# Performance work log

Measured on AMD Instinct MI355X. Metric: run time of the kernel, lower is better.

The kernel has to match this reference:

```python
import jax, jax.numpy as jnp
import numpy as np

B, S, D = 4, 2048, 2048
D_INNER = max(128, D // 2)  # 1024, torch default d_inner
FO = 2                      # filter_order
K = 3                       # kernel_size
KS = 3                      # short_kernel_size


def setup_inputs() -> dict:
    key = jax.random.key(0)
    ks = jax.random.split(key, 6)
    return {
        "x": jax.random.normal(ks[0], (B, S, D), jnp.float32),
        # depthwise short conv: weight (D, KS), bias (D,)
        "short_w": jax.random.normal(ks[1], (D, KS), jnp.float32) / np.float32(np.sqrt(KS)),
        "short_b": jnp.zeros((D,), jnp.float32),
        # filter MLP proj: Linear(D -> FO*D_INNER)
        "proj_w": jax.random.normal(ks[2], (D, FO * D_INNER), jnp.float32) / np.float32(np.sqrt(D)),
        "proj_b": jnp.zeros((FO * D_INNER,), jnp.float32),
        # filter MLP output: Linear(D_INNER -> K), SHARED across filter orders
        "filt_w": jax.random.normal(ks[3], (D_INNER, K), jnp.float32) / np.float32(np.sqrt(D_INNER)),
        "filt_b": jnp.zeros((K,), jnp.float32),
        # output projection Linear(D -> D)
        "out_w": jax.random.normal(ks[4], (D, D), jnp.float32) / np.float32(np.sqrt(D)),
        "out_b": jnp.zeros((D,), jnp.float32),
    }


def reference(x, short_w, short_b, proj_w, proj_b, filt_w, filt_b, out_w, out_b):
    b, s, d = x.shape
    v = x  # v captured BEFORE short-conv residual, as in the torch code

    # --- causal depthwise short conv (pad k-1 on left, truncate to s) ---
    xp = jnp.pad(x, ((0, 0), (KS - 1, 0), (0, 0)))
    x_short = short_b
    for j in range(KS):  # tiny fixed kernel loop
        x_short = x_short + xp[:, j:j + s, :] * short_w[:, j]
    x = x + x_short

    # --- filter function: Linear -> GELU -> (shared) Linear -> tanh ---
    h = jax.nn.gelu(x @ proj_w + proj_b, approximate=False)         # (b, s, FO*D_INNER)
    h = h.reshape(b, s, FO, D_INNER)
    filt = jnp.tanh(jnp.einsum('bsfi,ik->bsfk', h, filt_w) + filt_b)  # (b, s, FO, K)

    # --- gated depthwise conv: kernel = mean over seq, shared across channels;
    # sum over filter orders commutes with the (linear) conv, so fold it in ---
    w = filt.mean(axis=1).sum(axis=1)                                # (b, K)
    xp2 = jnp.pad(x, ((0, 0), (K - 1, 0), (0, 0)))
    conv = jnp.zeros_like(x)
    for j in range(K):
        conv = conv + xp2[:, j:j + s, :] * w[:, j][:, None, None]

    # --- gate with v, GELU, output projection ---
    y = jax.nn.gelu(conv * v, approximate=False)
    return y @ out_w + out_b
```

## Files before the change

kernel.cpp:

```cpp
#include <hip/hip_runtime.h>
#include <hip/hip_bf16.h>
#include <math.h>

typedef unsigned short u16;
typedef __attribute__((ext_vector_type(4))) unsigned short u16x4;
typedef __attribute__((ext_vector_type(8))) unsigned short u16x8;
typedef __attribute__((ext_vector_type(8))) short s16x8;
typedef __attribute__((ext_vector_type(4))) float f32x4;

#define B_  4
#define S_  2048
#define D_  2048
#define DI_ 1024
#define MROWS (B_ * S_)
#define KDIM  D_
#define NDIM  D_

__device__ __forceinline__ float b2f(u16 u) {
    union { unsigned i; float f; } v; v.i = ((unsigned)u) << 16; return v.f;
}
__device__ __forceinline__ u16 f2b(float f) {
    unsigned u = __float_as_uint(f);
    unsigned r = (u + 0x7FFFu + ((u >> 16) & 1u)) >> 16;
    return (u16)r;
}
__device__ __forceinline__ float gelu_exact(float x) {
    return 0.5f * x * (1.0f + erff(x * 0.70710678118654752f));
}

#define GLOAD_LDS16(gp, lp)                                                    \
    __builtin_amdgcn_global_load_lds(                                          \
        (const __attribute__((address_space(1))) void*)(gp),                   \
        (__attribute__((address_space(3))) void*)(lp), 16, 0, 0)

__global__ void transpose_k(const float* __restrict__ in, u16* __restrict__ out, int n) {
    __shared__ float tile[32][33];
    int bx = blockIdx.x * 32, by = blockIdx.y * 32;
    int tx = threadIdx.x, ty = threadIdx.y;
    for (int i = 0; i < 32; i += 8)
        tile[ty + i][tx] = in[(size_t)(by + ty + i) * n + bx + tx];
    __syncthreads();
    for (int i = 0; i < 32; i += 8)
        out[(size_t)(bx + ty + i) * n + by + tx] = f2b(tile[tx][ty + i]);
}

__global__ void shortconv_k(const float* __restrict__ x, const float* __restrict__ sw,
                            const float* __restrict__ sb, u16* __restrict__ xs,
                            float* __restrict__ wacc) {
    if (blockIdx.x == 0 && threadIdx.x < 12) wacc[threadIdx.x] = 0.0f;
    int gid = blockIdx.x * 256 + threadIdx.x;
    int r = gid >> 9;
    int c = (gid & 511) << 2;
    int t = r & (S_ - 1);
    const float* base = x + (size_t)r * D_ + c;
    f32x4 cur = *(const f32x4*)base;
    f32x4 m1 = (t >= 1) ? *(const f32x4*)(base - D_) : (f32x4)(0.0f);
    f32x4 m2 = (t >= 2) ? *(const f32x4*)(base - 2 * D_) : (f32x4)(0.0f);
    u16x4 out;
    #pragma unroll
    for (int e = 0; e < 4; ++e) {
        int d = c + e;
        float v = cur[e] + sb[d]
                + sw[d * 3 + 0] * m2[e]
                + sw[d * 3 + 1] * m1[e]
                + sw[d * 3 + 2] * cur[e];
        out[e] = f2b(v);
    }
    *(u16x4*)(xs + (size_t)r * D_ + c) = out;
}

template <bool GELU, bool OUT_F32>
__global__ void gemm_k(const u16* __restrict__ A, const u16* __restrict__ BT,
                       const float* __restrict__ bias, void* __restrict__ Cv,
                       int M, int N, int K) {
    __shared__ u16 As[128 * 32];
    __shared__ u16 Bs[128 * 32];
    const int tid = threadIdx.x;
    const int wid = tid >> 6;
    const int lane = tid & 63;
    const int wm = (wid >> 1) * 64;
    const int wn = (wid & 1) * 64;
    const int row0 = blockIdx.y * 128;
    const int col0 = blockIdx.x * 128;

    f32x4 acc[4][4];
    #pragma unroll
    for (int i = 0; i < 4; ++i)
        #pragma unroll
        for (int j = 0; j < 4; ++j) acc[i][j] = (f32x4)(0.0f);

    const int srow_l = lane >> 2;
    const int sk = (lane & 3) * 8;

    const int mrow = wm + (lane & 15);
    const int nrow = wn + (lane & 15);
    const int k0 = (lane >> 4) * 8;

    for (int kt = 0; kt < K; kt += 32) {
        __syncthreads();
        #pragma unroll
        for (int p = 0; p < 2; ++p) {
            int srow = p * 64 + wid * 16 + srow_l;
            u16* lpa = &As[(p * 4 + wid) * 512];
            u16* lpb = &Bs[(p * 4 + wid) * 512];
            const u16* ga = A + (size_t)(row0 + srow) * K + kt + sk;
            const u16* gb = BT + (size_t)(col0 + srow) * K + kt + sk;
            GLOAD_LDS16(ga, lpa);
            GLOAD_LDS16(gb, lpb);
        }
        __syncthreads();

        s16x8 af[4], bfr[4];
        #pragma unroll
        for (int i = 0; i < 4; ++i)
            af[i] = *(const s16x8*)&As[(size_t)(mrow + i * 16) * 32 + k0];
        #pragma unroll
        for (int j = 0; j < 4; ++j)
            bfr[j] = *(const s16x8*)&Bs[(size_t)(nrow + j * 16) * 32 + k0];
        #pragma unroll
        for (int i = 0; i < 4; ++i)
            #pragma unroll
            for (int j = 0; j < 4; ++j)
                acc[i][j] = __builtin_amdgcn_mfma_f32_16x16x32_bf16(
                    af[i], bfr[j], acc[i][j], 0, 0, 0);
    }

    const int crow0 = row0 + wm + (lane >> 4) * 4;
    const int ccol0 = col0 + wn + (lane & 15);
    #pragma unroll
    for (int j = 0; j < 4; ++j) {
        int col = ccol0 + j * 16;
        float bs = bias[col];
        #pragma unroll
        for (int i = 0; i < 4; ++i) {
            int rbase = crow0 + i * 16;
            #pragma unroll
            for (int r = 0; r < 4; ++r) {
                float v = acc[i][j][r] + bs;
                if (GELU) v = gelu_exact(v);
                if (OUT_F32)
                    ((float*)Cv)[(size_t)(rbase + r) * N + col] = v;
                else
                    ((u16*)Cv)[(size_t)(rbase + r) * N + col] = f2b(v);
            }
        }
    }
}

__global__ void filt_reduce_k(const u16* __restrict__ h, const float* __restrict__ fw,
                              const float* __restrict__ fb, float* __restrict__ wacc) {
    __shared__ float part[3];
    const int tid = threadIdx.x;
    if (tid < 3) part[tid] = 0.0f;
    __syncthreads();
    const int wid = tid >> 6;
    const int lane = tid & 63;
    const int f = lane >> 5;
    const int j = lane & 31;

    float fwr[96];
    const f32x4* fp4 = (const f32x4*)(fw + (size_t)j * 96);
    #pragma unroll
    for (int e = 0; e < 24; ++e) ((f32x4*)fwr)[e] = fp4[e];
    const float fb0 = fb[0], fb1 = fb[1], fb2 = fb[2];

    const int row0 = blockIdx.x * 16 + wid * 4;
    #pragma unroll
    for (int rr = 0; rr < 4; ++rr) {
        int row = row0 + rr;
        const u16* hp = h + (size_t)row * D_ + f * DI_ + j * 32;
        u16x8 hv[4];
        hv[0] = *(const u16x8*)(hp);
        hv[1] = *(const u16x8*)(hp + 8);
        hv[2] = *(const u16x8*)(hp + 16);
        hv[3] = *(const u16x8*)(hp + 24);
        float t0 = 0.f, t1 = 0.f, t2 = 0.f;
        #pragma unroll
        for (int q = 0; q < 4; ++q)
            #pragma unroll
            for (int e = 0; e < 8; ++e) {
                float hf = b2f(hv[q][e]);
                int ib = (q * 8 + e) * 3;
                t0 += hf * fwr[ib + 0];
                t1 += hf * fwr[ib + 1];
                t2 += hf * fwr[ib + 2];
            }
        #pragma unroll
        for (int off = 16; off > 0; off >>= 1) {
            t0 += __shfl_down(t0, off, 32);
            t1 += __shfl_down(t1, off, 32);
            t2 += __shfl_down(t2, off, 32);
        }
        if (j == 0) {
            atomicAdd(&part[0], tanhf(t0 + fb0));
            atomicAdd(&part[1], tanhf(t1 + fb1));
            atomicAdd(&part[2], tanhf(t2 + fb2));
        }
    }
    __syncthreads();
    if (tid < 3) {
        int b = blockIdx.x >> 7;
        atomicAdd(&wacc[b * 3 + tid], part[tid]);
    }
}

__global__ void gate_k(const u16* __restrict__ xs, const float* __restrict__ v,
                       const float* __restrict__ wacc, u16* __restrict__ g) {
    int gid = blockIdx.x * 256 + threadIdx.x;
    int r = gid >> 9;
    int c = (gid & 511) << 2;
    int t = r & (S_ - 1);
    int b = r >> 11;
    float w0 = wacc[b * 3 + 0] * (1.0f / (float)S_);
    float w1 = wacc[b * 3 + 1] * (1.0f / (float)S_);
    float w2 = wacc[b * 3 + 2] * (1.0f / (float)S_);
    const u16* base = xs + (size_t)r * D_ + c;
    u16x4 cur = *(const u16x4*)base;
    u16x4 m1 = (t >= 1) ? *(const u16x4*)(base - D_) : (u16x4)(0);
    u16x4 m2 = (t >= 2) ? *(const u16x4*)(base - 2 * D_) : (u16x4)(0);
    f32x4 vv = *(const f32x4*)(v + (size_t)r * D_ + c);
    u16x4 out;
    #pragma unroll
    for (int e = 0; e < 4; ++e) {
        float conv = w0 * b2f(m2[e]) + w1 * b2f(m1[e]) + w2 * b2f(cur[e]);
        out[e] = f2b(gelu_exact(conv * vv[e]));
    }
    *(u16x4*)(g + (size_t)r * D_ + c) = out;
}

extern "C" void kernel_launch(void* const* d_in, const int* in_sizes, int n_in,
                              void* d_out, int out_size, void* d_ws, size_t ws_size,
                              hipStream_t stream) {
    const float* x       = (const float*)d_in[0];
    const float* short_w = (const float*)d_in[1];
    const float* short_b = (const float*)d_in[2];
    const float* proj_w  = (const float*)d_in[3];
    const float* proj_b  = (const float*)d_in[4];
    const float* filt_w  = (const float*)d_in[5];
    const float* filt_b  = (const float*)d_in[6];
    const float* out_w   = (const float*)d_in[7];
    const float* out_b   = (const float*)d_in[8];
    float* out = (float*)d_out;

    char* ws = (char*)d_ws;
    const size_t xs_bytes = (size_t)MROWS * D_ * 2;
    float* wacc = (float*)(ws);
    u16*   xs   = (u16*)(ws + 256);
    u16*   hg   = (u16*)(ws + 256 + xs_bytes);
    u16*   wT   = (u16*)(ws + 256 + 2 * xs_bytes);

    dim3 tb(32, 8, 1);
    dim3 tg(D_ / 32, D_ / 32, 1);
    transpose_k<<<tg, tb, 0, stream>>>(proj_w, wT, D_);

    int ew_blocks = (MROWS * D_ / 4) / 256;
    shortconv_k<<<ew_blocks, 256, 0, stream>>>(x, short_w, short_b, xs, wacc);

    dim3 gg(NDIM / 128, MROWS / 128, 1);
    gemm_k<true, false><<<gg, 256, 0, stream>>>(xs, wT, proj_b, hg, MROWS, NDIM, KDIM);

    filt_reduce_k<<<512, 256, 0, stream>>>(hg, filt_w, filt_b, wacc);

    transpose_k<<<tg, tb, 0, stream>>>(out_w, wT, D_);

    gate_k<<<ew_blocks, 256, 0, stream>>>(xs, x, wacc, hg);

    gemm_k<false, true><<<gg, 256, 0, stream>>>(hg, wT, out_b, out, MROWS, NDIM, KDIM);
}
```

Before: 400.8 us.

## Fuse GELU filter projection into first GEMM epilogue and swizzle LDS tiles

The first GEMM epilogue now applies GELU and immediately contracts against the shared filter weights. Partial sums are reduced per row in LDS and then atomically accumulated into a small per-row buffer. This removes the bf16 write and re-read of the full hidden activation, and a small kernel finishes the tanh and mean. Separately, LDS tile loads and reads use an XOR swizzle to reduce bank conflicts. The cost is extra shuffles and LDS and global atomics in the epilogue, and a different floating-point summation order.

```diff
diff --git a/kernel.cpp b/kernel.cpp
--- a/kernel.cpp
+++ b/kernel.cpp
@@ -46,8 +46,12 @@
 
 __global__ void shortconv_k(const float* __restrict__ x, const float* __restrict__ sw,
                             const float* __restrict__ sb, u16* __restrict__ xs,
-                            float* __restrict__ wacc) {
+                            float* __restrict__ wacc, float* __restrict__ t_g) {
     if (blockIdx.x == 0 && threadIdx.x < 12) wacc[threadIdx.x] = 0.0f;
+    if (blockIdx.x < 192) {
+        int z = blockIdx.x * 256 + threadIdx.x;
+        t_g[z] = 0.0f;
+    }
     int gid = blockIdx.x * 256 + threadIdx.x;
     int r = gid >> 9;
     int c = (gid & 511) << 2;
@@ -69,12 +73,14 @@
     *(u16x4*)(xs + (size_t)r * D_ + c) = out;
 }
 
-template <bool GELU, bool OUT_F32>
+template <bool FILT>
 __global__ void gemm_k(const u16* __restrict__ A, const u16* __restrict__ BT,
-                       const float* __restrict__ bias, void* __restrict__ Cv,
+                       const float* __restrict__ bias, float* __restrict__ C,
+                       const float* __restrict__ fw, float* __restrict__ t_g,
                        int M, int N, int K) {
     __shared__ u16 As[128 * 32];
     __shared__ u16 Bs[128 * 32];
+    __shared__ float t_lds[128 * 3];
     const int tid = threadIdx.x;
     const int wid = tid >> 6;
     const int lane = tid & 63;
@@ -83,6 +89,10 @@
     const int row0 = blockIdx.y * 128;
     const int col0 = blockIdx.x * 128;
 
+    if (FILT) {
+        for (int z = tid; z < 384; z += 256) t_lds[z] = 0.0f;
+    }
+
     f32x4 acc[4][4];
     #pragma unroll
     for (int i = 0; i < 4; ++i)
@@ -90,21 +100,22 @@
         for (int j = 0; j < 4; ++j) acc[i][j] = (f32x4)(0.0f);
 
     const int srow_l = lane >> 2;
-    const int sk = (lane & 3) * 8;
+    const int cs = lane & 3;
 
     const int mrow = wm + (lane & 15);
     const int nrow = wn + (lane & 15);
-    const int k0 = (lane >> 4) * 8;
+    const int cf = lane >> 4;
 
     for (int kt = 0; kt < K; kt += 32) {
         __syncthreads();
         #pragma unroll
         for (int p = 0; p < 2; ++p) {
             int srow = p * 64 + wid * 16 + srow_l;
+            int gc = cs ^ ((srow >> 1) & 3);
             u16* lpa = &As[(p * 4 + wid) * 512];
             u16* lpb = &Bs[(p * 4 + wid) * 512];
-            const u16* ga = A + (size_t)(row0 + srow) * K + kt + sk;
-            const u16* gb = BT + (size_t)(col0 + srow) * K + kt + sk;
+            const u16* ga = A + (size_t)(row0 + srow) * K + kt + gc * 8;
+            const u16* gb = BT + (size_t)(col0 + srow) * K + kt + gc * 8;
             GLOAD_LDS16(ga, lpa);
             GLOAD_LDS16(gb, lpb);
         }
@@ -112,11 +123,15 @@
 
         s16x8 af[4], bfr[4];
         #pragma unroll
-        for (int i = 0; i < 4; ++i)
-            af[i] = *(const s16x8*)&As[(size_t)(mrow + i * 16) * 32 + k0];
-        #pragma unroll
-        for (int j = 0; j < 4; ++j)
-            bfr[j] = *(const s16x8*)&Bs[(size_t)(nrow + j * 16) * 32 + k0];
+        for (int i = 0; i < 4; ++i) {
+            int ra = mrow + i * 16;
+            af[i] = *(const s16x8*)&As[ra * 32 + ((cf ^ ((ra >> 1) & 3)) * 8)];
+        }
+        #pragma unroll
+        for (int j = 0; j < 4; ++j) {
+            int rb = nrow + j * 16;
+            bfr[j] = *(const s16x8*)&Bs[rb * 32 + ((cf ^ ((rb >> 1) & 3)) * 8)];
+        }
         #pragma unroll
         for (int i = 0; i < 4; ++i)
             #pragma unroll
@@ -125,81 +140,82 @@
                     af[i], bfr[j], acc[i][j], 0, 0, 0);
     }
 
-    const int crow0 = row0 + wm + (lane >> 4) * 4;
-    const int ccol0 = col0 + wn + (lane & 15);
-    #pragma unroll
-    for (int j = 0; j < 4; ++j) {
-        int col = ccol0 + j * 16;
-        float bs = bias[col];
+    const int colt0 = wn + (lane & 15);
+    if (FILT) {
+        float fwv[4][3], bsv[4];
+        const int ibase = (col0 & (DI_ - 1)) + colt0;
+        #pragma unroll
+        for (int j = 0; j < 4; ++j) {
+            int ifilt = ibase + j * 16;
+            fwv[j][0] = fw[ifilt * 3 + 0];
+            fwv[j][1] = fw[ifilt * 3 + 1];
+            fwv[j][2] = fw[ifilt * 3 + 2];
+            bsv[j] = bias[col0 + colt0 + j * 16];
+        }
         #pragma unroll
         for (int i = 0; i < 4; ++i) {
-            int rbase = crow0 + i * 16;
             #pragma unroll
             for (int r = 0; r < 4; ++r) {
-                float v = acc[i][j][r] + bs;
-                if (GELU) v = gelu_exact(v);
-                if (OUT_F32)
-                    ((float*)Cv)[(size_t)(rbase + r) * N + col] = v;
-                else
-                    ((u16*)Cv)[(size_t)(rbase + r) * N + col] = f2b(v);
+                float s0 = 0.f, s1 = 0.f, s2 = 0.f;
+                #pragma unroll
+                for (int j = 0; j < 4; ++j) {
+                    float hv = gelu_exact(acc[i][j][r] + bsv[j]);
+                    s0 += hv * fwv[j][0];
+                    s1 += hv * fwv[j][1];
+                    s2 += hv * fwv[j][2];
+                }
+                #pragma unroll
+                for (int m = 1; m < 16; m <<= 1) {
+                    s0 += __shfl_xor(s0, m, 16);
+                    s1 += __shfl_xor(s1, m, 16);
+                    s2 += __shfl_xor(s2, m, 16);
+                }
+                if ((lane & 15) == 0) {
+                    int trow = wm + (lane >> 4) * 4 + i * 16 + r;
+                    atomicAdd(&t_lds[trow * 3 + 0], s0);
+                    atomicAdd(&t_lds[trow * 3 + 1], s1);
+                    atomicAdd(&t_lds[trow * 3 + 2], s2);
+                }
             }
         }
-    }
-}
-
-__global__ void filt_reduce_k(const u16* __restrict__ h, const float* __restrict__ fw,
-                              const float* __restrict__ fb, float* __restrict__ wacc) {
+        __syncthreads();
+        const int f3 = (col0 >= DI_) ? 3 : 0;
+        for (int z = tid; z < 384; z += 256) {
+            int rr = z / 3, k = z - rr * 3;
+            atomicAdd(&t_g[(size_t)(row0 + rr) * 6 + f3 + k], t_lds[z]);
+        }
+    } else {
+        const int crow0 = row0 + wm + (lane >> 4) * 4;
+        #pragma unroll
+        for (int j = 0; j < 4; ++j) {
+            int col = col0 + colt0 + j * 16;
+            float bs = bias[col];
+            #pragma unroll
+            for (int i = 0; i < 4; ++i) {
+                int rbase = crow0 + i * 16;
+                #pragma unroll
+                for (int r = 0; r < 4; ++r)
+                    C[(size_t)(rbase + r) * N + col] = acc[i][j][r] + bs;
+            }
+        }
+    }
+}
+
+__global__ void filt_finish_k(const float* __restrict__ t_g, const float* __restrict__ fb,
+                              float* __restrict__ wacc) {
     __shared__ float part[3];
     const int tid = threadIdx.x;
     if (tid < 3) part[tid] = 0.0f;
     __syncthreads();
-    const int wid = tid >> 6;
-    const int lane = tid & 63;
-    const int f = lane >> 5;
-    const int j = lane & 31;
-
-    float fwr[96];
-    const f32x4* fp4 = (const f32x4*)(fw + (size_t)j * 96);
-    #pragma unroll
-    for (int e = 0; e < 24; ++e) ((f32x4*)fwr)[e] = fp4[e];
-    const float fb0 = fb[0], fb1 = fb[1], fb2 = fb[2];
-
-    const int row0 = blockIdx.x * 16 + wid * 4;
-    #pragma unroll
-    for (int rr = 0; rr < 4; ++rr) {
-        int row = row0 + rr;
-        const u16* hp = h + (size_t)row * D_ + f * DI_ + j * 32;
-        u16x8 hv[4];
-        hv[0] = *(const u16x8*)(hp);
-        hv[1] = *(const u16x8*)(hp + 8);
-        hv[2] = *(const u16x8*)(hp + 16);
-        hv[3] = *(const u16x8*)(hp + 24);
-        float t0 = 0.f, t1 = 0.f, t2 = 0.f;
-        #pragma unroll
-        for (int q = 0; q < 4; ++q)
-            #pragma unroll
-            for (int e = 0; e < 8; ++e) {
-                float hf = b2f(hv[q][e]);
-                int ib = (q * 8 + e) * 3;
-                t0 += hf * fwr[ib + 0];
-                t1 += hf * fwr[ib + 1];
-                t2 += hf * fwr[ib + 2];
-            }
-        #pragma unroll
-        for (int off = 16; off > 0; off >>= 1) {
-            t0 += __shfl_down(t0, off, 32);
-            t1 += __shfl_down(t1, off, 32);
-            t2 += __shfl_down(t2, off, 32);
-        }
-        if (j == 0) {
-            atomicAdd(&part[0], tanhf(t0 + fb0));
-            atomicAdd(&part[1], tanhf(t1 + fb1));
-            atomicAdd(&part[2], tanhf(t2 + fb2));
-        }
-    }
+    int p = blockIdx.x * 256 + tid;
+    int row = p >> 1, f = p & 1;
+    const float* tp = t_g + (size_t)row * 6 + f * 3;
+    atomicAdd(&part[0], tanhf(tp[0] + fb[0]));
+    atomicAdd(&part[1], tanhf(tp[1] + fb[1]));
+    atomicAdd(&part[2], tanhf(tp[2] + fb[2]));
     __syncthreads();
     if (tid < 3) {
-        int b = blockIdx.x >> 7;
+        int b = blockIdx.x >> 4;
         atomicAdd(&wacc[b * 3 + tid], part[tid]);
     }
 }
@@ -245,25 +261,28 @@
     char* ws = (char*)d_ws;
     const size_t xs_bytes = (size_t)MROWS * D_ * 2;
     float* wacc = (float*)(ws);
-    u16*   xs   = (u16*)(ws + 256);
-    u16*   hg   = (u16*)(ws + 256 + xs_bytes);
-    u16*   wT   = (u16*)(ws + 256 + 2 * xs_bytes);
+    float* t_g  = (float*)(ws + 1024);
+    u16*   xs   = (u16*)(ws + 262144);
+    u16*   g    = (u16*)(ws + 262144 + xs_bytes);
+    u16*   wT   = (u16*)(ws + 262144 + 2 * xs_bytes);
 
     dim3 tb(32, 8, 1);
     dim3 tg(D_ / 32, D_ / 32, 1);
     transpose_k<<<tg, tb, 0, stream>>>(proj_w, wT, D_);
 
     int ew_blocks = (MROWS * D_ / 4) / 256;
-    shortconv_k<<<ew_blocks, 256, 0, stream>>>(x, short_w, short_b, xs, wacc);
+    shortconv_k<<<ew_blocks, 256, 0, stream>>>(x, short_w, short_b, xs, wacc, t_g);
 
     dim3 gg(NDIM / 128, MROWS / 128, 1);
-    gemm_k<true, false><<<gg, 256, 0, stream>>>(xs, wT, proj_b, hg, MROWS, NDIM, KDIM);
-
-    filt_reduce_k<<<512, 256, 0, stream>>>(hg, filt_w, filt_b, wacc);
+    gemm_k<true><<<gg, 256, 0, stream>>>(xs, wT, proj_b, nullptr, filt_w, t_g,
+                                         MROWS, NDIM, KDIM);
+
+    filt_finish_k<<<64, 256, 0, stream>>>(t_g, filt_b, wacc);
 
     transpose_k<<<tg, tb, 0, stream>>>(out_w, wT, D_);
 
-    gate_k<<<ew_blocks, 256, 0, stream>>>(xs, x, wacc, hg);
-
-    gemm_k<false, true><<<gg, 256, 0, stream>>>(hg, wT, out_b, out, MROWS, NDIM, KDIM);
-}
+    gate_k<<<ew_blocks, 256, 0, stream>>>(xs, x, wacc, g);
+
+    gemm_k<false><<<gg, 256, 0, stream>>>(g, wT, out_b, out, nullptr, nullptr,
+                                          MROWS, NDIM, KDIM);
+}
```

Measured after the change: 392.7 us. 1.02x faster.
